# Optimization experiments

Measured on AMD Instinct MI355X. Metric: run time of the kernel, lower is better.

The kernel has to match this reference:

```python
import jax, jax.numpy as jnp
import numpy as np

WS, SS, NH = 7, 3, 3  # window_size, shift_size, num_heads


def window_partition(x, ws):
    B, H, W, C = x.shape
    x = x.reshape(B, H // ws, ws, W // ws, ws, C)
    return jnp.transpose(x, (0, 1, 3, 2, 4, 5)).reshape(-1, ws, ws, C)


def window_reverse(w, ws, H, W):
    B = w.shape[0] // (H * W // ws // ws)
    x = w.reshape(B, H // ws, W // ws, ws, ws, -1)
    return jnp.transpose(x, (0, 1, 3, 2, 4, 5)).reshape(B, H, W, -1)


def layernorm(x, scale, bias, eps=1e-6):
    mu = x.mean(-1, keepdims=True)
    var = ((x - mu) ** 2).mean(-1, keepdims=True)
    return (x - mu) * jax.lax.rsqrt(var + eps) * scale + bias


def make_attn_mask(Hp, Wp, ws, ss):
    # static (trace-time) shifted-window mask, (nW, N, N)
    img = np.zeros((1, Hp, Wp, 1), np.float32)
    cnt = 0
    for h in (slice(0, -ws), slice(-ws, -ss), slice(-ss, None)):
        for w in (slice(0, -ws), slice(-ws, -ss), slice(-ss, None)):
            img[:, h, w, :] = cnt
            cnt += 1
    mw = img.reshape(1, Hp // ws, ws, Wp // ws, ws, 1).transpose(0, 1, 3, 2, 4, 5).reshape(-1, ws * ws)
    am = mw[:, None, :] - mw[:, :, None]
    return np.where(am != 0, -100.0, 0.0).astype(np.float32)


def setup_inputs() -> dict:
    key = jax.random.key(0)
    ks = jax.random.split(key, 8)
    B, H, W, C = 4, 56, 56, 96
    s = lambda k, shape: jax.random.normal(k, shape, jnp.float32) * 0.02
    return {
        'x': jax.random.normal(ks[0], (B, H * W, C), jnp.float32),
        'Hp': H, 'Wp': W,
        'norm1_scale': jnp.ones((C,), jnp.float32), 'norm1_bias': jnp.zeros((C,), jnp.float32),
        'qkv_w': s(ks[1], (C, 3 * C)), 'qkv_b': jnp.zeros((3 * C,), jnp.float32),
        'proj_w': s(ks[2], (C, C)), 'proj_b': jnp.zeros((C,), jnp.float32),
        'tb_ln1_scale': jnp.ones((C,), jnp.float32), 'tb_ln1_bias': jnp.zeros((C,), jnp.float32),
        'tb_qkv_w': s(ks[3], (C, 3 * C)), 'tb_qkv_b': jnp.zeros((3 * C,), jnp.float32),
        'tb_out_w': s(ks[4], (C, C)), 'tb_out_b': jnp.zeros((C,), jnp.float32),
        'tb_ln2_scale': jnp.ones((C,), jnp.float32), 'tb_ln2_bias': jnp.zeros((C,), jnp.float32),
        'tb_fc1_w': s(ks[5], (C, 4 * C)), 'tb_fc1_b': jnp.zeros((4 * C,), jnp.float32),
        'tb_fc2_w': s(ks[6], (4 * C, C)), 'tb_fc2_b': jnp.zeros((C,), jnp.float32),
    }


def reference(x, Hp, Wp, norm1_scale, norm1_bias, qkv_w, qkv_b, proj_w, proj_b,
              tb_ln1_scale, tb_ln1_bias, tb_qkv_w, tb_qkv_b, tb_out_w, tb_out_b,
              tb_ln2_scale, tb_ln2_bias, tb_fc1_w, tb_fc1_b, tb_fc2_w, tb_fc2_b):
    ws, ss, nh = WS, SS, NH
    B, L, C = x.shape
    H, W = int(Hp), int(Wp)
    hd = C // nh
    shortcut = x
    h = layernorm(x, norm1_scale, norm1_bias).reshape(B, H, W, C)
    pad_r = (ws - W % ws) % ws
    pad_b = (ws - H % ws) % ws
    h = jnp.pad(h, ((0, 0), (0, pad_b), (0, pad_r), (0, 0)))
    Hpad, Wpad = H + pad_b, W + pad_r
    shifted = jnp.roll(h, (-ss, -ss), (1, 2))
    attn_mask = jnp.asarray(make_attn_mask(Hpad, Wpad, ws, ss))  # (nW, N, N)
    xw = window_partition(shifted, ws).reshape(-1, ws * ws, C)  # (B*nW, N, C)
    Bw, N, _ = xw.shape
    qkv = (xw @ qkv_w + qkv_b).reshape(Bw, N, 3, nh, hd).transpose(2, 0, 3, 1, 4)
    q, k, v = qkv[0], qkv[1], qkv[2]
    attn = jnp.einsum('bhnd,bhmd->bhnm', q, k) * hd ** -0.5
    nW = attn_mask.shape[0]
    attn = attn.reshape(Bw // nW, nW, nh, N, N) + attn_mask[None, :, None]
    attn = jax.nn.softmax(attn.reshape(-1, nh, N, N), axis=-1)
    out = jnp.einsum('bhnm,bhmd->bhnd', attn, v).transpose(0, 2, 1, 3).reshape(Bw, N, C)
    out = out @ proj_w + proj_b
    out = window_reverse(out.reshape(-1, ws, ws, C), ws, Hpad, Wpad)
    out = jnp.roll(out, (ss, ss), (1, 2))[:, :H, :W, :].reshape(B, H * W, C)
    x = shortcut + out
    # trailing pre-LN transformer block: global MHSA + MLP
    y = layernorm(x, tb_ln1_scale, tb_ln1_bias)
    qkv2 = (y @ tb_qkv_w + tb_qkv_b).reshape(B, L, 3, nh, hd).transpose(2, 0, 3, 1, 4)
    q2, k2, v2 = qkv2[0], qkv2[1], qkv2[2]
    a2 = jax.nn.softmax(jnp.einsum('bhnd,bhmd->bhnm', q2, k2) * hd ** -0.5, axis=-1)
    ao = jnp.einsum('bhnm,bhmd->bhnd', a2, v2).transpose(0, 2, 1, 3).reshape(B, L, C)
    x = x + (ao @ tb_out_w + tb_out_b)
    z = layernorm(x, tb_ln2_scale, tb_ln2_bias)
    z = jax.nn.gelu(z @ tb_fc1_w + tb_fc1_b) @ tb_fc2_w + tb_fc2_b
    x = x + z
    return (x, H, W)
```

## Files before the change

kernel.cpp:

```cpp
#include <hip/hip_runtime.h>
#include <hip/hip_bf16.h>

#define CD 96
#define LROW 3136
#define QSCALE 0.17677669529663687f
#define LOG2E 1.4426950408889634f
#define MASKLOG2 -144.26950408889634f

using f32x4 = __attribute__((ext_vector_type(4))) float;
using bf8   = __attribute__((ext_vector_type(8))) short;

__device__ __forceinline__ short f2bf(float f) {
  union { float f; unsigned u; } v; v.f = f;
  unsigned r = v.u + 0x7fffu + ((v.u >> 16) & 1u);
  return (short)(r >> 16);
}
__device__ __forceinline__ float bf2f(unsigned short s) {
  return __uint_as_float((unsigned)s << 16);
}
__device__ __forceinline__ unsigned pack_bf2(float lo, float hi) {
  return (__float_as_uint(hi) & 0xffff0000u) | (__float_as_uint(lo) >> 16);
}
__device__ __forceinline__ unsigned pack_bf2r(float lo, float hi) {
  return ((unsigned)(unsigned short)f2bf(hi) << 16) | (unsigned short)f2bf(lo);
}
__device__ __forceinline__ float fast_exp2(float x) {
  return __builtin_amdgcn_exp2f(x);
}

#define GLOAD_LDS16(src, dst) \
  __builtin_amdgcn_global_load_lds((const __attribute__((address_space(1))) void*)(src), \
                                   (__attribute__((address_space(3))) void*)(dst), 16, 0, 0)

__global__ __launch_bounds__(256) void ln_kernel(const float* __restrict__ x,
                                                 const float* __restrict__ g,
                                                 const float* __restrict__ b,
                                                 short* __restrict__ out, int rows) {
  int slot = threadIdx.x >> 5, l32 = threadIdx.x & 31;
  int row = blockIdx.x * 8 + slot;
  if (row >= rows) return;
  const float* xr = x + (size_t)row * CD + l32 * 3;
  float a0 = xr[0], a1 = xr[1], a2 = xr[2];
  float s = a0 + a1 + a2;
#pragma unroll
  for (int off = 16; off >= 1; off >>= 1) s += __shfl_xor(s, off, 32);
  float mu = s * (1.f / 96.f);
  float d0 = a0 - mu, d1 = a1 - mu, d2 = a2 - mu;
  float q = d0 * d0 + d1 * d1 + d2 * d2;
#pragma unroll
  for (int off = 16; off >= 1; off >>= 1) q += __shfl_xor(q, off, 32);
  float rstd = rsqrtf(q * (1.f / 96.f) + 1e-6f);
  int c0 = l32 * 3;
  short* orow = out + (size_t)row * CD + c0;
  orow[0] = f2bf(d0 * rstd * g[c0] + b[c0]);
  orow[1] = f2bf(d1 * rstd * g[c0 + 1] + b[c0 + 1]);
  orow[2] = f2bf(d2 * rstd * g[c0 + 2] + b[c0 + 2]);
}

__global__ __launch_bounds__(256) void cvt_wt_kernel(const float* __restrict__ W,
                                                     short* __restrict__ Wt,
                                                     int K, int N, int Npad) {
  int idx = blockIdx.x * 256 + threadIdx.x;
  if (idx >= Npad * K) return;
  int nr = idx / K, kk = idx - nr * K;
  float v = (nr < N) ? W[(size_t)kk * N + nr] : 0.f;
  Wt[idx] = f2bf(v);
}

__global__ __launch_bounds__(512) void win_attn_kernel(
    const short* __restrict__ hb, const float* __restrict__ xin,
    const short* __restrict__ wwin, const float* __restrict__ qkv_b,
    const short* __restrict__ wproj, const float* __restrict__ proj_b,
    float* __restrict__ x1) {
  __shared__ __align__(16) short Xs[64][104];
  __shared__ __align__(16) short Qs[3][64][40];
  __shared__ __align__(16) short Ks[3][64][40];
  __shared__ __align__(16) short Vt[3][32][72];
  __shared__ __align__(16) short Os[64][104];
  __shared__ __align__(16) short Ptw[8][16][72];
  __shared__ int cnt[64];
  __shared__ int gidx[49];

  int tid = threadIdx.x, lane = tid & 63, wid = tid >> 6;
  int lr = lane & 15, lg = lane >> 4;
  int b = blockIdx.x >> 6, w64 = blockIdx.x & 63;
  int wr = w64 >> 3, wc = w64 & 7;

  if (tid < 64) {
    if (tid < 49) {
      int i = tid / 7, j = tid % 7;
      int sh = wr * 7 + i, sw = wc * 7 + j;
      int hr = (sh < 49) ? 0 : ((sh < 53) ? 1 : 2);
      int wreg = (sw < 49) ? 0 : ((sw < 53) ? 1 : 2);
      cnt[tid] = hr * 3 + wreg;
      gidx[tid] = ((sh + 3) % 56) * 56 + ((sw + 3) % 56);
    } else {
      cnt[tid] = -1;
    }
  }
  __syncthreads();

  for (int c = tid; c < 768; c += 512) {
    int row = c / 12, cc = c % 12;
    uint4 v = {0u, 0u, 0u, 0u};
    if (row < 49) v = *reinterpret_cast<const uint4*>(hb + ((size_t)b * LROW + gidx[row]) * 96 + cc * 8);
    *reinterpret_cast<uint4*>(&Xs[row][cc * 8]) = v;
  }
  __syncthreads();

  for (int nt = wid; nt < 18; nt += 8) {
    f32x4 acc[4];
#pragma unroll
    for (int mi = 0; mi < 4; ++mi) acc[mi] = (f32x4){0.f, 0.f, 0.f, 0.f};
#pragma unroll
    for (int kc = 0; kc < 3; ++kc) {
      bf8 bfr = *reinterpret_cast<const bf8*>(wwin + (size_t)(nt * 16 + lr) * 96 + kc * 32 + lg * 8);
#pragma unroll
      for (int mi = 0; mi < 4; ++mi) {
        bf8 afr = *reinterpret_cast<const bf8*>(&Xs[mi * 16 + lr][kc * 32 + lg * 8]);
        acc[mi] = __builtin_amdgcn_mfma_f32_16x16x32_bf16(afr, bfr, acc[mi], 0, 0, 0);
      }
    }
    int n = nt * 16 + lr;
    int sec = n / 96, within = n % 96;
    int hh = within >> 5, dd = within & 31;
    float bias = qkv_b[n];
#pragma unroll
    for (int mi = 0; mi < 4; ++mi)
#pragma unroll
      for (int r = 0; r < 4; ++r) {
        int mrow = mi * 16 + lg * 4 + r;
        float v = acc[mi][r] + bias;
        if (sec == 0)      Qs[hh][mrow][dd] = f2bf(v * (QSCALE * LOG2E));
        else if (sec == 1) Ks[hh][mrow][dd] = f2bf(v);
        else               Vt[hh][dd][mrow] = f2bf(v);
      }
  }
  __syncthreads();

  int cntkv[16];
#pragma unroll
  for (int t = 0; t < 4; ++t)
#pragma unroll
    for (int r = 0; r < 4; ++r) cntkv[t * 4 + r] = cnt[t * 16 + lg * 4 + r];

  for (int p = wid; p < 12; p += 8) {
    int h = p >> 2, qt = p & 3;
    bf8 qf = *reinterpret_cast<const bf8*>(&Qs[h][qt * 16 + lr][lg * 8]);
    int cq = cnt[qt * 16 + lr];
    f32x4 z = {0.f, 0.f, 0.f, 0.f};
    f32x4 St[4];
    __builtin_amdgcn_s_setprio(1);
#pragma unroll
    for (int t = 0; t < 4; ++t) {
      bf8 kf = *reinterpret_cast<const bf8*>(&Ks[h][t * 16 + lr][lg * 8]);
      St[t] = __builtin_amdgcn_mfma_f32_16x16x32_bf16(kf, qf, z, 0, 0, 0);
    }
    __builtin_amdgcn_s_setprio(0);
    float rs = 0.f;
#pragma unroll
    for (int t = 0; t < 4; ++t)
#pragma unroll
      for (int r = 0; r < 4; ++r) {
        float a = St[t][r] + ((cq == cntkv[t * 4 + r]) ? 0.f : MASKLOG2);
        float pp = fast_exp2(a);
        St[t][r] = pp;
        rs += pp;
      }
    rs += __shfl_xor(rs, 16);
    rs += __shfl_xor(rs, 32);
    float inv = 1.f / rs;
#pragma unroll
    for (int t = 0; t < 4; ++t) {
      uint2 w;
      w.x = pack_bf2(St[t][0], St[t][1]);
      w.y = pack_bf2(St[t][2], St[t][3]);
      *reinterpret_cast<uint2*>(&Ptw[wid][lr][t * 16 + lg * 4]) = w;
    }
    f32x4 O0 = {0.f, 0.f, 0.f, 0.f}, O1 = {0.f, 0.f, 0.f, 0.f};
    __builtin_amdgcn_s_setprio(1);
#pragma unroll
    for (int c = 0; c < 2; ++c) {
      bf8 pbf = *reinterpret_cast<const bf8*>(&Ptw[wid][lr][c * 32 + lg * 8]);
      bf8 v0 = *reinterpret_cast<const bf8*>(&Vt[h][lr][c * 32 + lg * 8]);
      bf8 v1 = *reinterpret_cast<const bf8*>(&Vt[h][16 + lr][c * 32 + lg * 8]);
      O0 = __builtin_amdgcn_mfma_f32_16x16x32_bf16(v0, pbf, O0, 0, 0, 0);
      O1 = __builtin_amdgcn_mfma_f32_16x16x32_bf16(v1, pbf, O1, 0, 0, 0);
    }
    __builtin_amdgcn_s_setprio(0);
#pragma unroll
    for (int r = 0; r < 4; ++r) {
      Os[qt * 16 + lr][h * 32 + lg * 4 + r] = f2bf(O0[r] * inv);
      Os[qt * 16 + lr][h * 32 + 16 + lg * 4 + r] = f2bf(O1[r] * inv);
    }
  }
  __syncthreads();

  int mt = wid & 3, half = wid >> 2;
  int gi[4];
#pragma unroll
  for (int r = 0; r < 4; ++r) {
    int q = mt * 16 + lg * 4 + r;
    gi[r] = (q < 49) ? gidx[q] : -1;
  }
  for (int nt = half * 3; nt < half * 3 + 3; ++nt) {
    f32x4 acc = {0.f, 0.f, 0.f, 0.f};
#pragma unroll
    for (int kc = 0; kc < 3; ++kc) {
      bf8 afr = *reinterpret_cast<const bf8*>(&Os[mt * 16 + lr][kc * 32 + lg * 8]);
      bf8 bfr = *reinterpret_cast<const bf8*>(wproj + (size_t)(nt * 16 + lr) * 96 + kc * 32 + lg * 8);
      acc = __builtin_amdgcn_mfma_f32_16x16x32_bf16(afr, bfr, acc, 0, 0, 0);
    }
    int n = nt * 16 + lr;
    float pb = proj_b[n];
#pragma unroll
    for (int r = 0; r < 4; ++r) {
      if (gi[r] >= 0) {
        size_t rowo = ((size_t)b * LROW + gi[r]) * CD + n;
        x1[rowo] = acc[r] + pb + xin[rowo];
      }
    }
  }
}

template <int MODE>
__global__ __launch_bounds__(256) void gemm_mfma_kernel(
    const short* __restrict__ A, const short* __restrict__ Bt,
    const float* __restrict__ bias, const float* __restrict__ res,
    void* __restrict__ outp, int M, int K, int N) {
  __shared__ __align__(16) short As[2][128 * 32];
  __shared__ __align__(16) short Bs[2][64 * 32];
  int tid = threadIdx.x, lane = tid & 63, wid = tid >> 6;
  int lr = lane & 15, lg = lane >> 4;
  int m0 = blockIdx.x * 128, n0 = blockIdx.y * 64;
  int nk = K >> 5;

  f32x4 acc[2][4];
#pragma unroll
  for (int i = 0; i < 2; ++i)
#pragma unroll
    for (int j = 0; j < 4; ++j) acc[i][j] = (f32x4){0.f, 0.f, 0.f, 0.f};

  auto stage = [&](int bf, int ks) {
    int k0 = ks * 32;
#pragma unroll
    for (int p = 0; p < 2; ++p) {
      int idx = tid + p * 256;
      GLOAD_LDS16(A + (size_t)(m0 + (idx >> 2)) * K + k0 + (idx & 3) * 8,
                  &As[bf][idx * 8]);
    }
    GLOAD_LDS16(Bt + (size_t)(n0 + (tid >> 2)) * K + k0 + (tid & 3) * 8,
                &Bs[bf][tid * 8]);
  };

  stage(0, 0);
  __syncthreads();
  int buf = 0;
  for (int ks = 0; ks < nk; ++ks) {
    if (ks + 1 < nk) stage(buf ^ 1, ks + 1);
    bf8 bfr[4], afr[2];
#pragma unroll
    for (int ni = 0; ni < 4; ++ni)
      bfr[ni] = *reinterpret_cast<const bf8*>(&Bs[buf][(ni * 16 + lr) * 32 + lg * 8]);
#pragma unroll
    for (int mi = 0; mi < 2; ++mi)
      afr[mi] = *reinterpret_cast<const bf8*>(&As[buf][(wid * 32 + mi * 16 + lr) * 32 + lg * 8]);
    __builtin_amdgcn_s_setprio(1);
#pragma unroll
    for (int mi = 0; mi < 2; ++mi)
#pragma unroll
      for (int ni = 0; ni < 4; ++ni)
        acc[mi][ni] = __builtin_amdgcn_mfma_f32_16x16x32_bf16(afr[mi], bfr[ni], acc[mi][ni], 0, 0, 0);
    __builtin_amdgcn_s_setprio(0);
    __syncthreads();
    buf ^= 1;
  }

#pragma unroll
  for (int mi = 0; mi < 2; ++mi)
#pragma unroll
    for (int ni = 0; ni < 4; ++ni)
#pragma unroll
      for (int r = 0; r < 4; ++r) {
        int mrow = m0 + wid * 32 + mi * 16 + lg * 4 + r;
        int n = n0 + ni * 16 + lr;
        if (n < N) {
          float v = acc[mi][ni][r] + bias[n];
          if (MODE == 0) {
            float t = tanhf(0.7978845608028654f * (v + 0.044715f * v * v * v));
            ((short*)outp)[(size_t)mrow * N + n] = f2bf(0.5f * v * (1.f + t));
          } else {
            v += res[(size_t)mrow * N + n];
            ((float*)outp)[(size_t)mrow * N + n] = v;
          }
        }
      }
}

__global__ __launch_bounds__(256) void qkv_mfma_kernel(
    const short* __restrict__ A, const short* __restrict__ Bt,
    const float* __restrict__ bias,
    short* __restrict__ qb, short* __restrict__ kb, short* __restrict__ vtb) {
  __shared__ __align__(16) short As[2][128 * 32];
  __shared__ __align__(16) short Bs[2][64 * 32];
  int tid = threadIdx.x, lane = tid & 63, wid = tid >> 6;
  int lr = lane & 15, lg = lane >> 4;
  int m0 = blockIdx.x * 128, n0 = blockIdx.y * 64;
  const int K = 96;

  f32x4 acc[2][4];
#pragma unroll
  for (int i = 0; i < 2; ++i)
#pragma unroll
    for (int j = 0; j < 4; ++j) acc[i][j] = (f32x4){0.f, 0.f, 0.f, 0.f};

  auto stage = [&](int bf, int ks) {
    int k0 = ks * 32;
#pragma unroll
    for (int p = 0; p < 2; ++p) {
      int idx = tid + p * 256;
      GLOAD_LDS16(A + (size_t)(m0 + (idx >> 2)) * K + k0 + (idx & 3) * 8,
                  &As[bf][idx * 8]);
    }
    GLOAD_LDS16(Bt + (size_t)(n0 + (tid >> 2)) * K + k0 + (tid & 3) * 8,
                &Bs[bf][tid * 8]);
  };

  stage(0, 0);
  __syncthreads();
  int buf = 0;
  for (int ks = 0; ks < 3; ++ks) {
    if (ks + 1 < 3) stage(buf ^ 1, ks + 1);
    bf8 bfr[4], afr[2];
#pragma unroll
    for (int ni = 0; ni < 4; ++ni)
      bfr[ni] = *reinterpret_cast<const bf8*>(&Bs[buf][(ni * 16 + lr) * 32 + lg * 8]);
#pragma unroll
    for (int mi = 0; mi < 2; ++mi)
      afr[mi] = *reinterpret_cast<const bf8*>(&As[buf][(wid * 32 + mi * 16 + lr) * 32 + lg * 8]);
    __builtin_amdgcn_s_setprio(1);
#pragma unroll
    for (int mi = 0; mi < 2; ++mi)
#pragma unroll
      for (int ni = 0; ni < 4; ++ni)
        acc[mi][ni] = __builtin_amdgcn_mfma_f32_16x16x32_bf16(afr[mi], bfr[ni], acc[mi][ni], 0, 0, 0);
    __builtin_amdgcn_s_setprio(0);
    __syncthreads();
    buf ^= 1;
  }

#pragma unroll
  for (int mi = 0; mi < 2; ++mi)
#pragma unroll
    for (int ni = 0; ni < 4; ++ni)
#pragma unroll
      for (int r = 0; r < 4; ++r) {
        int mrow = m0 + wid * 32 + mi * 16 + lg * 4 + r;
        int n = n0 + ni * 16 + lr;
        if (n < 288) {
          float v = acc[mi][ni][r] + bias[n];
          int sec = n / 96, within = n % 96;
          int hh = within >> 5, dd = within & 31;
          int bb = mrow / LROW, nn = mrow - bb * LROW;
          size_t bh = (size_t)bb * 3 + hh;
          if (sec == 0)      qb[(bh * LROW + nn) * 32 + dd] = f2bf(v * (QSCALE * LOG2E));
          else if (sec == 1) kb[(bh * LROW + nn) * 32 + dd] = f2bf(v);
          else               vtb[(bh * 32 + dd) * LROW + nn] = f2bf(v);
        }
      }
}

__global__ __launch_bounds__(128) void flash_mfma_kernel(
    const short* __restrict__ qb, const short* __restrict__ kb,
    const short* __restrict__ vtb,
    short* __restrict__ pOb, float* __restrict__ pl) {
  __shared__ __align__(16) short Pt[2][2][16][72];
  int tid = threadIdx.x, lane = tid & 63, wid = tid >> 6;
  int lr = lane & 15, lg = lane >> 4;
  int bh = blockIdx.y, s = blockIdx.z;
  int q0 = blockIdx.x * 64 + wid * 32;
  const short* qbb = qb + (size_t)bh * LROW * 32;
  const short* kbase = kb + (size_t)bh * LROW * 32 + lr * 32 + lg * 8;
  const short* vbase = vtb + (size_t)bh * 32 * LROW + lr * LROW + lg * 8;

  bf8 qf0 = *reinterpret_cast<const bf8*>(qbb + (size_t)(q0 + lr) * 32 + lg * 8);
  bf8 qf1 = *reinterpret_cast<const bf8*>(qbb + (size_t)(q0 + 16 + lr) * 32 + lg * 8);

  f32x4 O00 = {0.f,0.f,0.f,0.f}, O01 = {0.f,0.f,0.f,0.f};
  f32x4 O10 = {0.f,0.f,0.f,0.f}, O11 = {0.f,0.f,0.f,0.f};
  float l0v = 0.f, l1v = 0.f;

  const int tbl[5] = {0, 13, 25, 37, 49};
  int t0 = tbl[s], t1 = tbl[s + 1];

  bf8 kA[4], vA[4], kB[4], vB[4];

  auto loadt = [&](bf8 (&Kf)[4], bf8 (&Vf)[4], int kt) {
    const short* kp = kbase + (size_t)kt * 2048;
#pragma unroll
    for (int t = 0; t < 4; ++t) Kf[t] = *reinterpret_cast<const bf8*>(kp + t * 512);
    const short* vp = vbase + kt * 64;
#pragma unroll
    for (int c = 0; c < 2; ++c) {
      Vf[c]     = *reinterpret_cast<const bf8*>(vp + c * 32);
      Vf[2 + c] = *reinterpret_cast<const bf8*>(vp + 16 * LROW + c * 32);
    }
  };

  auto body = [&](bf8 (&Kf)[4], bf8 (&Vf)[4]) {
    f32x4 z = {0.f, 0.f, 0.f, 0.f};
#pragma unroll
    for (int g = 0; g < 2; ++g) {
      bf8 qf = g ? qf1 : qf0;
      float& lgv = g ? l1v : l0v;
      f32x4 St[4];
      __builtin_amdgcn_s_setprio(1);
#pragma unroll
      for (int t = 0; t < 4; ++t)
        St[t] = __builtin_amdgcn_mfma_f32_16x16x32_bf16(Kf[t], qf, z, 0, 0, 0);
      __builtin_amdgcn_s_setprio(0);
      float rs = 0.f;
#pragma unroll
      for (int t = 0; t < 4; ++t)
#pragma unroll
        for (int r = 0; r < 4; ++r) {
          float p = fast_exp2(St[t][r]);
          St[t][r] = p;
          rs += p;
        }
      rs += __shfl_xor(rs, 16);
      rs += __shfl_xor(rs, 32);
      lgv += rs;
#pragma unroll
      for (int t = 0; t < 4; ++t) {
        uint2 w;
        w.x = pack_bf2(St[t][0], St[t][1]);
        w.y = pack_bf2(St[t][2], St[t][3]);
        *reinterpret_cast<uint2*>(&Pt[wid][g][lr][t * 16 + lg * 4]) = w;
      }
    }
    __builtin_amdgcn_s_setprio(1);
#pragma unroll
    for (int g = 0; g < 2; ++g) {
      f32x4& Oh0 = g ? O10 : O00;
      f32x4& Oh1 = g ? O11 : O01;
#pragma unroll
      for (int c = 0; c < 2; ++c) {
        bf8 pbf = *reinterpret_cast<const bf8*>(&Pt[wid][g][lr][c * 32 + lg * 8]);
        Oh0 = __builtin_amdgcn_mfma_f32_16x16x32_bf16(Vf[c], pbf, Oh0, 0, 0, 0);
        Oh1 = __builtin_amdgcn_mfma_f32_16x16x32_bf16(Vf[2 + c], pbf, Oh1, 0, 0, 0);
      }
    }
    __builtin_amdgcn_s_setprio(0);
  };

  loadt(kA, vA, t0);
  int kt = t0;
  for (; kt + 2 <= t1 - 1; kt += 2) {
    loadt(kB, vB, kt + 1);
    body(kA, vA);
    loadt(kA, vA, kt + 2);
    body(kB, vB);
  }
  if (kt < t1 - 1) {
    loadt(kB, vB, kt + 1);
    body(kA, vA);
    body(kB, vB);
  } else {
    body(kA, vA);
  }

  size_t rbase = (size_t)(s * 12 + bh) * LROW;
  size_t r0 = (rbase + q0 + lr) * 32;
  size_t r1 = (rbase + q0 + 16 + lr) * 32;
  uint2 w;
  w.x = pack_bf2r(O00[0], O00[1]); w.y = pack_bf2r(O00[2], O00[3]);
  *reinterpret_cast<uint2*>(&pOb[r0 + lg * 4]) = w;
  w.x = pack_bf2r(O01[0], O01[1]); w.y = pack_bf2r(O01[2], O01[3]);
  *reinterpret_cast<uint2*>(&pOb[r0 + 16 + lg * 4]) = w;
  w.x = pack_bf2r(O10[0], O10[1]); w.y = pack_bf2r(O10[2], O10[3]);
  *reinterpret_cast<uint2*>(&pOb[r1 + lg * 4]) = w;
  w.x = pack_bf2r(O11[0], O11[1]); w.y = pack_bf2r(O11[2], O11[3]);
  *reinterpret_cast<uint2*>(&pOb[r1 + 16 + lg * 4]) = w;
  if (lg == 0) {
    pl[rbase + q0 + lr] = l0v;
    pl[rbase + q0 + 16 + lr] = l1v;
  }
}

__global__ __launch_bounds__(256) void flash_merge_kernel(
    const short* __restrict__ pOb, const float* __restrict__ pl,
    short* __restrict__ aob) {
  int idx = blockIdx.x * 256 + threadIdx.x;
  int d = idx & 31, row = idx >> 5;
  const int NR = 12 * LROW;
  float o = 0.f, l = 0.f;
#pragma unroll
  for (int s = 0; s < 4; ++s) {
    o += bf2f((unsigned short)pOb[(size_t)s * NR * 32 + idx]);
    l += pl[(size_t)s * NR + row];
  }
  int bh = row / LROW, q = row - bh * LROW;
  int b = bh / 3, h = bh - b * 3;
  aob[((size_t)b * LROW + q) * CD + h * 32 + d] = f2bf(o / l);
}

__global__ void tail_kernel(const int* __restrict__ Hp, const int* __restrict__ Wp,
                            float* __restrict__ o) {
  o[0] = (float)Hp[0];
  o[1] = (float)Wp[0];
}

extern "C" void kernel_launch(void* const* d_in, const int* in_sizes, int n_in,
                              void* d_out, int out_size, void* d_ws, size_t ws_size,
                              hipStream_t stream) {
  const float* x      = (const float*)d_in[0];
  const int*   Hp     = (const int*)d_in[1];
  const int*   Wp     = (const int*)d_in[2];
  const float* n1s    = (const float*)d_in[3];
  const float* n1b    = (const float*)d_in[4];
  const float* qkv_w  = (const float*)d_in[5];
  const float* qkv_b  = (const float*)d_in[6];
  const float* proj_w = (const float*)d_in[7];
  const float* proj_b = (const float*)d_in[8];
  const float* ln1s   = (const float*)d_in[9];
  const float* ln1b   = (const float*)d_in[10];
  const float* qkv2_w = (const float*)d_in[11];
  const float* qkv2_b = (const float*)d_in[12];
  const float* out_w  = (const float*)d_in[13];
  const float* out_b  = (const float*)d_in[14];
  const float* ln2s   = (const float*)d_in[15];
  const float* ln2b   = (const float*)d_in[16];
  const float* fc1_w  = (const float*)d_in[17];
  const float* fc1_b  = (const float*)d_in[18];
  const float* fc2_w  = (const float*)d_in[19];
  const float* fc2_b  = (const float*)d_in[20];

  float* wsf = (float*)d_ws;
  const size_t U = (size_t)4 * LROW * CD;
  float* x1   = wsf;
  float* x2   = wsf + U;
  short* hb   = (short*)(wsf + 2 * U);
  short* tb   = (short*)(wsf + 2 * U + U / 2);
  short* qb   = (short*)(wsf + 4 * U + U / 2);
  short* kb   = qb + U;
  short* vtb  = kb + U;
  short* wqkv = (short*)(wsf + 6 * U);
  short* wout = wqkv + 320 * 96;
  short* wfc1 = wout + 128 * 96;
  short* wfc2 = wfc1 + 384 * 96;
  short* wwin = wfc2 + 128 * 384;
  short* wproj = wwin + 288 * 96;
  short* pOb  = (short*)(wsf + U);
  float* pl   = wsf + 3 * U;
  short* aob  = qb;
  float* outx = (float*)d_out;

  const int M = 4 * LROW;

  cvt_wt_kernel<<<(320 * 96 + 255) / 256, 256, 0, stream>>>(qkv2_w, wqkv, 96, 288, 320);
  cvt_wt_kernel<<<(128 * 96 + 255) / 256, 256, 0, stream>>>(out_w, wout, 96, 96, 128);
  cvt_wt_kernel<<<(384 * 96 + 255) / 256, 256, 0, stream>>>(fc1_w, wfc1, 96, 384, 384);
  cvt_wt_kernel<<<(128 * 384 + 255) / 256, 256, 0, stream>>>(fc2_w, wfc2, 384, 96, 128);
  cvt_wt_kernel<<<(288 * 96 + 255) / 256, 256, 0, stream>>>(qkv_w, wwin, 96, 288, 288);
  cvt_wt_kernel<<<(96 * 96 + 255) / 256, 256, 0, stream>>>(proj_w, wproj, 96, 96, 96);

  ln_kernel<<<M / 8, 256, 0, stream>>>(x, n1s, n1b, hb, M);
  win_attn_kernel<<<256, 512, 0, stream>>>(hb, x, wwin, qkv_b, wproj, proj_b, x1);
  ln_kernel<<<M / 8, 256, 0, stream>>>(x1, ln1s, ln1b, hb, M);
  qkv_mfma_kernel<<<dim3(M / 128, 5), 256, 0, stream>>>(hb, wqkv, qkv2_b, qb, kb, vtb);
  flash_mfma_kernel<<<dim3(49, 12, 4), 128, 0, stream>>>(qb, kb, vtb, pOb, pl);
  flash_merge_kernel<<<12 * LROW * 32 / 256, 256, 0, stream>>>(pOb, pl, aob);
  gemm_mfma_kernel<1><<<dim3(M / 128, 2), 256, 0, stream>>>(aob, wout, out_b, x1, x2, M, 96, 96);
  ln_kernel<<<M / 8, 256, 0, stream>>>(x2, ln2s, ln2b, hb, M);
  gemm_mfma_kernel<0><<<dim3(M / 128, 6), 256, 0, stream>>>(hb, wfc1, fc1_b, nullptr, tb, M, 96, 384);
  gemm_mfma_kernel<1><<<dim3(M / 128, 2), 256, 0, stream>>>(tb, wfc2, fc2_b, x2, outx, M, 384, 96);
  tail_kernel<<<1, 1, 0, stream>>>(Hp, Wp, outx + U);
}
```

Measured before the change: 134.2 us.

## Split flash attention KV into six chunks, fuse weight conversions, tree-sum softmax

Raises the flash-decoding KV split from 4 to 6 chunks, so the global attention launches more blocks and each block runs a shorter serial loop. The merge kernel now sums 6 partials, and the partial-sum buffer is moved to make room. The six weight-conversion launches become one kernel that branches on index, cutting launch overhead. Softmax row sums use a pairwise tree instead of a serial chain to shorten the dependency chain. The trade-off is more partial-result traffic and merge work.

```diff
diff --git a/kernel.cpp b/kernel.cpp
--- a/kernel.cpp
+++ b/kernel.cpp
@@ -57,14 +57,23 @@
   orow[2] = f2bf(d2 * rstd * g[c0 + 2] + b[c0 + 2]);
 }
 
-__global__ __launch_bounds__(256) void cvt_wt_kernel(const float* __restrict__ W,
-                                                     short* __restrict__ Wt,
-                                                     int K, int N, int Npad) {
+__global__ __launch_bounds__(256) void cvt_all_kernel(
+    const float* __restrict__ qkv2_w, const float* __restrict__ out_w,
+    const float* __restrict__ fc1_w, const float* __restrict__ fc2_w,
+    const float* __restrict__ qkv_w, const float* __restrict__ proj_w,
+    short* __restrict__ dst) {
   int idx = blockIdx.x * 256 + threadIdx.x;
-  if (idx >= Npad * K) return;
-  int nr = idx / K, kk = idx - nr * K;
+  if (idx >= 165888) return;
+  const float* W; int K, N, off;
+  if (idx < 30720)       { W = qkv2_w; K = 96;  N = 288; off = idx; }
+  else if (idx < 43008)  { W = out_w;  K = 96;  N = 96;  off = idx - 30720; }
+  else if (idx < 79872)  { W = fc1_w;  K = 96;  N = 384; off = idx - 43008; }
+  else if (idx < 129024) { W = fc2_w;  K = 384; N = 96;  off = idx - 79872; }
+  else if (idx < 156672) { W = qkv_w;  K = 96;  N = 288; off = idx - 129024; }
+  else                   { W = proj_w; K = 96;  N = 96;  off = idx - 156672; }
+  int nr = off / K, kk = off - nr * K;
   float v = (nr < N) ? W[(size_t)kk * N + nr] : 0.f;
-  Wt[idx] = f2bf(v);
+  dst[idx] = f2bf(v);
 }
 
 __global__ __launch_bounds__(512) void win_attn_kernel(
@@ -157,16 +166,17 @@
       St[t] = __builtin_amdgcn_mfma_f32_16x16x32_bf16(kf, qf, z, 0, 0, 0);
     }
     __builtin_amdgcn_s_setprio(0);
-    float rs = 0.f;
-#pragma unroll
-    for (int t = 0; t < 4; ++t)
-#pragma unroll
-      for (int r = 0; r < 4; ++r) {
-        float a = St[t][r] + ((cq == cntkv[t * 4 + r]) ? 0.f : MASKLOG2);
-        float pp = fast_exp2(a);
-        St[t][r] = pp;
-        rs += pp;
-      }
+    float pr[4];
+#pragma unroll
+    for (int t = 0; t < 4; ++t) {
+      float p0 = fast_exp2(St[t][0] + ((cq == cntkv[t * 4 + 0]) ? 0.f : MASKLOG2));
+      float p1 = fast_exp2(St[t][1] + ((cq == cntkv[t * 4 + 1]) ? 0.f : MASKLOG2));
+      float p2 = fast_exp2(St[t][2] + ((cq == cntkv[t * 4 + 2]) ? 0.f : MASKLOG2));
+      float p3 = fast_exp2(St[t][3] + ((cq == cntkv[t * 4 + 3]) ? 0.f : MASKLOG2));
+      St[t][0] = p0; St[t][1] = p1; St[t][2] = p2; St[t][3] = p3;
+      pr[t] = (p0 + p1) + (p2 + p3);
+    }
+    float rs = (pr[0] + pr[1]) + (pr[2] + pr[3]);
     rs += __shfl_xor(rs, 16);
     rs += __shfl_xor(rs, 32);
     float inv = 1.f / rs;
@@ -390,7 +400,7 @@
   f32x4 O10 = {0.f,0.f,0.f,0.f}, O11 = {0.f,0.f,0.f,0.f};
   float l0v = 0.f, l1v = 0.f;
 
-  const int tbl[5] = {0, 13, 25, 37, 49};
+  const int tbl[7] = {0, 9, 17, 25, 33, 41, 49};
   int t0 = tbl[s], t1 = tbl[s + 1];
 
   bf8 kA[4], vA[4], kB[4], vB[4];
@@ -419,15 +429,17 @@
       for (int t = 0; t < 4; ++t)
         St[t] = __builtin_amdgcn_mfma_f32_16x16x32_bf16(Kf[t], qf, z, 0, 0, 0);
       __builtin_amdgcn_s_setprio(0);
-      float rs = 0.f;
-#pragma unroll
-      for (int t = 0; t < 4; ++t)
-#pragma unroll
-        for (int r = 0; r < 4; ++r) {
-          float p = fast_exp2(St[t][r]);
-          St[t][r] = p;
-          rs += p;
-        }
+      float pr[4];
+#pragma unroll
+      for (int t = 0; t < 4; ++t) {
+        float p0 = fast_exp2(St[t][0]);
+        float p1 = fast_exp2(St[t][1]);
+        float p2 = fast_exp2(St[t][2]);
+        float p3 = fast_exp2(St[t][3]);
+        St[t][0] = p0; St[t][1] = p1; St[t][2] = p2; St[t][3] = p3;
+        pr[t] = (p0 + p1) + (p2 + p3);
+      }
+      float rs = (pr[0] + pr[1]) + (pr[2] + pr[3]);
       rs += __shfl_xor(rs, 16);
       rs += __shfl_xor(rs, 32);
       lgv += rs;
@@ -496,7 +508,7 @@
   const int NR = 12 * LROW;
   float o = 0.f, l = 0.f;
 #pragma unroll
-  for (int s = 0; s < 4; ++s) {
+  for (int s = 0; s < 6; ++s) {
     o += bf2f((unsigned short)pOb[(size_t)s * NR * 32 + idx]);
     l += pl[(size_t)s * NR + row];
   }
@@ -545,31 +557,27 @@
   short* qb   = (short*)(wsf + 4 * U + U / 2);
   short* kb   = qb + U;
   short* vtb  = kb + U;
-  short* wqkv = (short*)(wsf + 6 * U);
+  short* wall = (short*)(wsf + 6 * U);
+  short* wqkv = wall;
   short* wout = wqkv + 320 * 96;
   short* wfc1 = wout + 128 * 96;
   short* wfc2 = wfc1 + 384 * 96;
   short* wwin = wfc2 + 128 * 384;
   short* wproj = wwin + 288 * 96;
   short* pOb  = (short*)(wsf + U);
-  float* pl   = wsf + 3 * U;
+  float* pl   = wsf + 4 * U;
   short* aob  = qb;
   float* outx = (float*)d_out;
 
   const int M = 4 * LROW;
 
-  cvt_wt_kernel<<<(320 * 96 + 255) / 256, 256, 0, stream>>>(qkv2_w, wqkv, 96, 288, 320);
-  cvt_wt_kernel<<<(128 * 96 + 255) / 256, 256, 0, stream>>>(out_w, wout, 96, 96, 128);
-  cvt_wt_kernel<<<(384 * 96 + 255) / 256, 256, 0, stream>>>(fc1_w, wfc1, 96, 384, 384);
-  cvt_wt_kernel<<<(128 * 384 + 255) / 256, 256, 0, stream>>>(fc2_w, wfc2, 384, 96, 128);
-  cvt_wt_kernel<<<(288 * 96 + 255) / 256, 256, 0, stream>>>(qkv_w, wwin, 96, 288, 288);
-  cvt_wt_kernel<<<(96 * 96 + 255) / 256, 256, 0, stream>>>(proj_w, wproj, 96, 96, 96);
+  cvt_all_kernel<<<(165888 + 255) / 256, 256, 0, stream>>>(qkv2_w, out_w, fc1_w, fc2_w, qkv_w, proj_w, wall);
 
   ln_kernel<<<M / 8, 256, 0, stream>>>(x, n1s, n1b, hb, M);
   win_attn_kernel<<<256, 512, 0, stream>>>(hb, x, wwin, qkv_b, wproj, proj_b, x1);
   ln_kernel<<<M / 8, 256, 0, stream>>>(x1, ln1s, ln1b, hb, M);
   qkv_mfma_kernel<<<dim3(M / 128, 5), 256, 0, stream>>>(hb, wqkv, qkv2_b, qb, kb, vtb);
-  flash_mfma_kernel<<<dim3(49, 12, 4), 128, 0, stream>>>(qb, kb, vtb, pOb, pl);
+  flash_mfma_kernel<<<dim3(49, 12, 6), 128, 0, stream>>>(qb, kb, vtb, pOb, pl);
   flash_merge_kernel<<<12 * LROW * 32 / 256, 256, 0, stream>>>(pOb, pl, aob);
   gemm_mfma_kernel<1><<<dim3(M / 128, 2), 256, 0, stream>>>(aob, wout, out_b, x1, x2, M, 96, 96);
   ln_kernel<<<M / 8, 256, 0, stream>>>(x2, ln2s, ln2b, hb, M);
```

After: 123.3 us. -8.1%, faster.
